# Kernel optimization log

Measured on AMD Instinct MI355X. Metric: run time of the kernel, lower is better.

The kernel has to match this reference:

```python
import jax, jax.numpy as jnp
import numpy as np
from itertools import product

C_IN, C_OUT = 32, 64
L, T = 96, 8            # 4D grid: 96^3 spatial x 8 time
EPS = 1e-5


def _build_maps():
    """Build sparse coords and MinkowskiEngine-style kernel maps (numpy, host side)."""
    rng = np.random.default_rng(0)
    n_cand = 400000
    coords = np.stack([rng.integers(0, L, n_cand), rng.integers(0, L, n_cand),
                       rng.integers(0, L, n_cand), rng.integers(0, T, n_cand)], axis=1).astype(np.int64)
    coords = np.unique(coords, axis=0)          # [n_in, 4] unique occupied voxels
    n_in = coords.shape[0]
    # --- downsample conv: kernel_size == stride == 2 -> each input hits exactly one output
    out_coords, inv = np.unique(coords // 2, axis=0, return_inverse=True)
    n_down = out_coords.shape[0]
    off_id = ((coords[:, 0] & 1) << 3) | ((coords[:, 1] & 1) << 2) | ((coords[:, 2] & 1) << 1) | (coords[:, 3] & 1)
    g, s = [], []
    for k in range(16):
        idx = np.nonzero(off_id == k)[0]
        g.append(idx); s.append(inv[idx])
    md = max(len(a) for a in g)
    gather_d = np.full((16, md), n_in, np.int32)    # dummy -> zero pad row of input feats
    scatter_d = np.full((16, md), n_down, np.int32)  # dummy -> trash output row
    for k in range(16):
        gather_d[k, :len(g[k])] = g[k]; scatter_d[k, :len(s[k])] = s[k]
    # --- refine conv: kernel 3, stride 1 on downsampled grid (same in/out coords)
    d0, d1 = L // 2, T // 2
    def enc(c):
        return ((c[:, 0] * d0 + c[:, 1]) * d0 + c[:, 2]) * d1 + c[:, 3]
    keys = enc(out_coords)
    order = np.argsort(keys)
    skeys = keys[order]
    g, s = [], []
    for off in product((-1, 0, 1), repeat=4):
        nb = out_coords + np.asarray(off)
        ok = (nb >= 0).all(1) & (nb[:, :3] < d0).all(1) & (nb[:, 3] < d1)
        nk = enc(np.where(ok[:, None], nb, 0))
        pos = np.clip(np.searchsorted(skeys, nk), 0, n_down - 1)
        hit = ok & (skeys[pos] == nk)
        g.append(order[pos[hit]]); s.append(np.nonzero(hit)[0])
    mr = max(len(a) for a in g)
    gather_r = np.full((81, mr), n_down, np.int32)
    scatter_r = np.full((81, mr), n_down, np.int32)
    for k in range(81):
        gather_r[k, :len(g[k])] = g[k]; scatter_r[k, :len(s[k])] = s[k]
    return n_in, n_down, gather_d, scatter_d, gather_r, scatter_r


def setup_inputs() -> dict:
    n_in, n_down, gather_d, scatter_d, gather_r, scatter_r = _build_maps()
    ks = jax.random.split(jax.random.key(0), 12)
    feat = jax.random.normal(ks[0], (n_in, C_IN), jnp.float32)
    w_down = jax.random.normal(ks[1], (16, C_IN, C_OUT), jnp.float32) / np.float32(np.sqrt(16 * C_IN))
    w_ref = jax.random.normal(ks[2], (81, C_OUT, C_OUT), jnp.float32) / np.float32(np.sqrt(81 * C_OUT))
    gamma_d = jnp.abs(jax.random.normal(ks[3], (C_OUT,), jnp.float32)) + 0.5
    beta_d = jax.random.normal(ks[4], (C_OUT,), jnp.float32) * 0.1
    mean_d = jax.random.normal(ks[5], (C_OUT,), jnp.float32) * 0.1
    var_d = jax.random.uniform(ks[6], (C_OUT,), jnp.float32, 0.5, 1.5)
    gamma_r = jnp.abs(jax.random.normal(ks[7], (C_OUT,), jnp.float32)) + 0.5
    beta_r = jax.random.normal(ks[8], (C_OUT,), jnp.float32) * 0.1
    mean_r = jax.random.normal(ks[9], (C_OUT,), jnp.float32) * 0.1
    var_r = jax.random.uniform(ks[10], (C_OUT,), jnp.float32, 0.5, 1.5)
    return {"feat": feat, "w_down": w_down, "gamma_d": gamma_d, "beta_d": beta_d,
            "mean_d": mean_d, "var_d": var_d, "w_ref": w_ref, "gamma_r": gamma_r,
            "beta_r": beta_r, "mean_r": mean_r, "var_r": var_r,
            "gather_d": jnp.asarray(gather_d), "scatter_d": jnp.asarray(scatter_d),
            "gather_r": jnp.asarray(gather_r), "scatter_r": jnp.asarray(scatter_r),
            "n_down": int(n_down)}


def _spconv_bn_relu(feat, w, gather, scatter, n_out, gamma, beta, mean, var):
    # gather-GEMM-scatter sparse conv, then eval-mode BN, then ReLU
    featp = jnp.concatenate([feat, jnp.zeros((1, feat.shape[1]), feat.dtype)], axis=0)
    out = jnp.zeros((n_out + 1, w.shape[-1]), feat.dtype)
    for k in range(w.shape[0]):        # fixed small set of kernel offsets (16 or 81)
        out = out.at[scatter[k]].add(featp[gather[k]] @ w[k])
    inv = gamma * jax.lax.rsqrt(var + EPS)
    return jax.nn.relu(out[:n_out] * inv + (beta - mean * inv))


def reference(feat, w_down, gamma_d, beta_d, mean_d, var_d, w_ref, gamma_r, beta_r,
              mean_r, var_r, gather_d, scatter_d, gather_r, scatter_r, n_down):
    n_down = int(n_down)
    y = _spconv_bn_relu(feat, w_down, gather_d, scatter_d, n_down, gamma_d, beta_d, mean_d, var_d)
    y = _spconv_bn_relu(y, w_ref, gather_r, scatter_r, n_down, gamma_r, beta_r, mean_r, var_r)
    return y
```

## Files before the change

kernel.cpp:

```cpp
#include <hip/hip_runtime.h>
#include <hip/hip_bf16.h>
#include <cstdint>

#define EPS_BN 1e-5f

typedef __attribute__((ext_vector_type(8)))  short bf16x8;
typedef __attribute__((ext_vector_type(16))) float f32x16;
typedef __attribute__((ext_vector_type(4)))  unsigned short u16x4;

#define MFMA32(a, b, c) __builtin_amdgcn_mfma_f32_32x32x16_bf16(a, b, c, 0, 0, 0)

#define GLOAD_LDS16(gsrc, ldst) \
    __builtin_amdgcn_global_load_lds((const __attribute__((address_space(1))) void*)(gsrc), \
                                     (__attribute__((address_space(3))) void*)(ldst), 16, 0, 0)

__global__ void build_inv(const int* __restrict__ gather, const int* __restrict__ scatter,
                          long total, int m, int* __restrict__ invT, int n_down) {
    long i = (long)blockIdx.x * blockDim.x + threadIdx.x;
    if (i >= total) return;
    int s = scatter[i];
    if (s < n_down) {
        int k = (int)(i / m);
        invT[(long)k * n_down + s] = gather[i];
    }
}

__global__ void build_invP(const int* __restrict__ gather, const int* __restrict__ scatter,
                           long total, int m, int* __restrict__ invP, int n_down, int nb64) {
    long i = (long)blockIdx.x * blockDim.x + threadIdx.x;
    if (i >= total) return;
    int s = scatter[i];
    if (s < n_down) {
        int k = (int)(i / m);
        int r = s & 63;
        int pos = ((r >> 5) << 5) + ((r & 7) << 2) + ((r >> 3) & 3);
        invP[(size_t)k * nb64 + ((size_t)(s >> 6) << 6) + pos] = gather[i];
    }
}

__global__ void fcvt(const float* __restrict__ f, unsigned short* __restrict__ fb,
                     unsigned short* __restrict__ ybf_pad, long n_in) {
    long t = (long)blockIdx.x * blockDim.x + threadIdx.x;
    long e = t * 4;
    long total = n_in * 32;
    if (e < total) {
        float4 v = *(const float4*)(f + e);
        u16x4 o;
        __hip_bfloat16 h;
        h = __float2bfloat16(v.x); o.x = *(unsigned short*)&h;
        h = __float2bfloat16(v.y); o.y = *(unsigned short*)&h;
        h = __float2bfloat16(v.z); o.z = *(unsigned short*)&h;
        h = __float2bfloat16(v.w); o.w = *(unsigned short*)&h;
        *(u16x4*)(fb + e) = o;
    } else if (e < total + 32) {
        u16x4 z = {0, 0, 0, 0};
        *(u16x4*)(fb + e) = z;
    }
    if (blockIdx.x == 0 && threadIdx.x < 16) {
        u16x4 z = {0, 0, 0, 0};
        ((u16x4*)ybf_pad)[threadIdx.x] = z;
    }
}

__global__ void wcvt_r(const float* __restrict__ w, unsigned short* __restrict__ wt) {
    int e = blockIdx.x * 256 + threadIdx.x;
    int k = e >> 12, r = e & 4095;
    int cin = ((r >> 10) << 4) + (r & 15);
    int col = (r >> 4) & 63;
    __hip_bfloat16 h = __float2bfloat16(w[(k << 12) + (cin << 6) + col]);
    wt[e] = *(unsigned short*)&h;
}

__global__ void wcvt_d(const float* __restrict__ w, unsigned short* __restrict__ wt) {
    int e = blockIdx.x * 256 + threadIdx.x;
    int k = e >> 11, r = e & 2047;
    int cin = ((r >> 10) << 4) + (r & 15);
    int col = (r >> 4) & 63;
    __hip_bfloat16 h = __float2bfloat16(w[(k << 11) + (cin << 6) + col]);
    wt[e] = *(unsigned short*)&h;
}

__global__ __launch_bounds__(256, 4) void conv_down_mfma(
        const unsigned short* __restrict__ fb, const unsigned short* __restrict__ wtd,
        const int* __restrict__ invd,
        const float* __restrict__ gamma, const float* __restrict__ beta,
        const float* __restrict__ mean, const float* __restrict__ var,
        unsigned short* __restrict__ y, int n_down, int n_in) {
    int  tid  = threadIdx.x;
    int  lane = tid & 63, l31 = lane & 31, lhi = lane >> 5;
    long wv   = ((long)blockIdx.x * 256 + tid) >> 6;
    long o0   = wv * 32;
    if (o0 >= n_down) return;

    int  oA = (int)(o0 + l31 < n_down ? o0 + l31 : n_down - 1);
    const short* ysb = (const short*)fb;

#define LDI_D(k) invd[(size_t)(k) * n_down + oA]
#define GATH_D(dst, g) { \
        const short* p = ysb + (size_t)((g) < 0 ? n_in : (g)) * 32 + lhi * 8; \
        dst[0] = *(const bf16x8*)p; dst[1] = *(const bf16x8*)(p + 16); }

    int g0 = LDI_D(0), gq1 = LDI_D(1), gq2 = LDI_D(2);
    bf16x8 ac[2];
    GATH_D(ac, g0);
    f32x16 acc0 = {}, acc1 = {};
    const short* wp = (const short*)wtd + l31 * 16 + lhi * 8;

    for (int k = 0; k < 16; ++k) {
        int gN = (k < 13) ? LDI_D(k + 3) : -1;
        bf16x8 an[2];
        GATH_D(an, gq1);
        const short* wk = wp + k * 2048;
#pragma unroll
        for (int kq = 0; kq < 2; ++kq) {
            bf16x8 b0 = *(const bf16x8*)(wk + kq * 1024);
            bf16x8 b1 = *(const bf16x8*)(wk + kq * 1024 + 512);
            acc0 = MFMA32(ac[kq], b0, acc0);
            acc1 = MFMA32(ac[kq], b1, acc1);
        }
        ac[0] = an[0]; ac[1] = an[1];
        gq1 = gq2; gq2 = gN;
    }

#pragma unroll
    for (int n = 0; n < 2; ++n) {
        int col = n * 32 + l31;
        float iv = gamma[col] * rsqrtf(var[col] + EPS_BN);
        float bb = beta[col] - mean[col] * iv;
        const f32x16& A = n ? acc1 : acc0;
#pragma unroll
        for (int i = 0; i < 16; ++i) {
            long oo = o0 + (i & 3) + 8 * (i >> 2) + 4 * lhi;
            if (oo < n_down) {
                __hip_bfloat16 h = __float2bfloat16(fmaxf(A[i] * iv + bb, 0.f));
                y[oo * 64 + col] = *(unsigned short*)&h;
            }
        }
    }
#undef LDI_D
#undef GATH_D
}

__global__ __launch_bounds__(256, 2) void conv_ref_mfma(
        const unsigned short* __restrict__ ybf, const unsigned short* __restrict__ wt,
        const int* __restrict__ invP,
        const float* __restrict__ gamma, const float* __restrict__ beta,
        const float* __restrict__ mean, const float* __restrict__ var,
        float* __restrict__ out, int n_down, int nb64, int nwg) {
    __shared__ char ldsA[4][2][8192];

    int bid = blockIdx.x;
    int q = nwg >> 3, r = nwg & 7;
    int xcd = bid & 7, pos = bid >> 3;
    int swzb = (xcd < r ? xcd * (q + 1) : r * (q + 1) + (xcd - r) * q) + pos;

    const int tid  = threadIdx.x;
    const int lane = tid & 63, l31 = lane & 31, lhi = lane >> 5;
    const int wid  = tid >> 6;
    const long o0  = ((long)swzb * 4 + wid) * 64;
    if (o0 >= n_down) return;

    const int  ro    = lane >> 3;
    const char* ybase = (const char*)ybf;
    char* ldsw = &ldsA[wid][0][0];
    const int swz = (((lane & 7) ^ ro) << 4);

    const char* ibase = (const char*)invP + (size_t)o0 * 4 + (size_t)ro * 16;

#define IDXP(k, S) { const char* p_ = ibase + (size_t)(k) * ((size_t)nb64 * 4); \
        S##a = *(const int4*)p_; S##b = *(const int4*)(p_ + 128); }

#define GL1(qv, BUF, i) { size_t g_ = (size_t)((qv) < 0 ? n_down : (qv)); \
        GLOAD_LDS16(ybase + g_ * 128 + swz, ldsw + (BUF) * 8192 + (i) * 1024); }

#define STAGE(BUF, S) { \
        GL1(S##a.x, BUF, 0); GL1(S##a.y, BUF, 1); GL1(S##a.z, BUF, 2); GL1(S##a.w, BUF, 3); \
        GL1(S##b.x, BUF, 4); GL1(S##b.y, BUF, 5); GL1(S##b.z, BUF, 6); GL1(S##b.w, BUF, 7); }

#define LDB(B0, B1, k) { \
        const short* wk_ = wp + (size_t)(k) * 4096; \
        _Pragma("unroll") \
        for (int kq = 0; kq < 4; ++kq) { \
            B0[kq] = *(const bf16x8*)(wk_ + kq * 1024); \
            B1[kq] = *(const bf16x8*)(wk_ + kq * 1024 + 512); } }

    const int rsw   = (l31 & 7) << 4;
    const int rowA  = l31 * 128, rowB = (32 + l31) * 128;
    const int lhi16 = lhi * 16;

#define COMPUTE(BUF, B0, B1) { \
        const char* la = ldsw + (BUF) * 8192; \
        __builtin_amdgcn_s_setprio(1); \
        _Pragma("unroll") \
        for (int kq = 0; kq < 4; ++kq) { \
            int fo = (kq * 32 + lhi16) ^ rsw; \
            bf16x8 aA = *(const bf16x8*)(la + rowA + fo); \
            bf16x8 aB = *(const bf16x8*)(la + rowB + fo); \
            acc0 = MFMA32(aA, B0[kq], acc0); \
            acc1 = MFMA32(aA, B1[kq], acc1); \
            acc2 = MFMA32(aB, B0[kq], acc2); \
            acc3 = MFMA32(aB, B1[kq], acc3); } \
        __builtin_amdgcn_s_setprio(0); }

#define REGION(CUR, NXT, S, kk, BC0, BC1, BN0, BN1) { \
        STAGE(NXT, S); \
        LDB(BN0, BN1, (kk) + 1); \
        IDXP((kk) + 4, S); \
        asm volatile("s_waitcnt vmcnt(20)" ::: "memory"); \
        __builtin_amdgcn_sched_barrier(0); \
        COMPUTE(CUR, BC0, BC1); }

    f32x16 acc0 = {}, acc1 = {}, acc2 = {}, acc3 = {};
    const short* wp = (const short*)wt + l31 * 16 + lhi * 8;
    bf16x8 B00[4], B01[4], B10[4], B11[4];
    int4 Ta, Tb, S0a, S0b, S1a, S1b, S2a, S2b;

    IDXP(0, T);
    IDXP(1, S0);
    IDXP(2, S1);
    IDXP(3, S2);
    asm volatile("s_waitcnt vmcnt(6)" ::: "memory");
    __builtin_amdgcn_sched_barrier(0);
    STAGE(0, T);
    LDB(B00, B01, 0);

    for (int k = 0; k < 78; k += 6) {
        REGION(0, 1, S0, k + 0, B00, B01, B10, B11);
        REGION(1, 0, S1, k + 1, B10, B11, B00, B01);
        REGION(0, 1, S2, k + 2, B00, B01, B10, B11);
        REGION(1, 0, S0, k + 3, B10, B11, B00, B01);
        REGION(0, 1, S1, k + 4, B00, B01, B10, B11);
        REGION(1, 0, S2, k + 5, B10, B11, B00, B01);
    }
    REGION(0, 1, S0, 78, B00, B01, B10, B11);
    REGION(1, 0, S1, 79, B10, B11, B00, B01);
    asm volatile("s_waitcnt vmcnt(2)" ::: "memory");
    __builtin_amdgcn_sched_barrier(0);
    COMPUTE(0, B00, B01);

#pragma unroll
    for (int m = 0; m < 2; ++m)
#pragma unroll
        for (int n = 0; n < 2; ++n) {
            int col = n * 32 + l31;
            float iv = gamma[col] * rsqrtf(var[col] + EPS_BN);
            float bb = beta[col] - mean[col] * iv;
            const f32x16& A = m == 0 ? (n == 0 ? acc0 : acc1) : (n == 0 ? acc2 : acc3);
#pragma unroll
            for (int i = 0; i < 16; ++i) {
                long oo = o0 + m * 32 + (i & 3) + 8 * (i >> 2) + 4 * lhi;
                if (oo < n_down)
                    out[oo * 64 + col] = fmaxf(A[i] * iv + bb, 0.f);
            }
        }
#undef IDXP
#undef GL1
#undef STAGE
#undef LDB
#undef COMPUTE
#undef REGION
}

extern "C" void kernel_launch(void* const* d_in, const int* in_sizes, int n_args,
                              void* d_out, int out_size, void* d_ws, size_t ws_size,
                              hipStream_t stream) {
    const float* feat    = (const float*)d_in[0];
    const float* w_down  = (const float*)d_in[1];
    const float* gamma_d = (const float*)d_in[2];
    const float* beta_d  = (const float*)d_in[3];
    const float* mean_d  = (const float*)d_in[4];
    const float* var_d   = (const float*)d_in[5];
    const float* w_ref   = (const float*)d_in[6];
    const float* gamma_r = (const float*)d_in[7];
    const float* beta_r  = (const float*)d_in[8];
    const float* mean_r  = (const float*)d_in[9];
    const float* var_r   = (const float*)d_in[10];
    const int*   gather_d  = (const int*)d_in[11];
    const int*   scatter_d = (const int*)d_in[12];
    const int*   gather_r  = (const int*)d_in[13];
    const int*   scatter_r = (const int*)d_in[14];

    int n_in   = in_sizes[0] / 32;
    int md     = in_sizes[11] / 16;
    int mr     = in_sizes[13] / 81;
    int n_down = out_size / 64;
    int nb64   = ((n_down + 63) / 64) * 64;

    char* ws = (char*)d_ws;
    size_t off = 0;
    auto alloc = [&](size_t bytes) { char* p = ws + off; off = (off + bytes + 255) & ~(size_t)255; return p; };
    unsigned short* ybf    = (unsigned short*)alloc((size_t)(n_down + 1) * 64 * 2);
    unsigned short* featbf = (unsigned short*)alloc((size_t)(n_in + 1) * 32 * 2);
    unsigned short* wt     = (unsigned short*)alloc((size_t)81 * 4096 * 2);
    unsigned short* wtd    = (unsigned short*)alloc((size_t)16 * 2048 * 2);
    int* invP = (int*)(ws + off);
    int* invd = invP + (size_t)84 * nb64;

    hipMemsetAsync(invP, 0xFF, ((size_t)84 * nb64 + (size_t)16 * n_down) * sizeof(int), stream);

    long td = 16L * md;
    build_inv<<<(int)((td + 255) / 256), 256, 0, stream>>>(gather_d, scatter_d, td, md, invd, n_down);
    long tr = 81L * mr;
    build_invP<<<(int)((tr + 255) / 256), 256, 0, stream>>>(gather_r, scatter_r, tr, mr, invP, n_down, nb64);

    long ft = ((long)n_in * 32 + 32) / 4;
    fcvt<<<(int)((ft + 255) / 256), 256, 0, stream>>>(feat, featbf, ybf + (size_t)n_down * 64, n_in);
    wcvt_r<<<81 * 4096 / 256, 256, 0, stream>>>(w_ref, wt);
    wcvt_d<<<16 * 2048 / 256, 256, 0, stream>>>(w_down, wtd);

    long wavesD  = ((long)n_down + 31) / 32;
    int  blocksD = (int)((wavesD * 64 + 255) / 256);
    conv_down_mfma<<<blocksD, 256, 0, stream>>>(featbf, wtd, invd,
                                                gamma_d, beta_d, mean_d, var_d,
                                                ybf, n_down, n_in);

    int blocksR = (n_down + 255) / 256;
    conv_ref_mfma<<<blocksR, 256, 0, stream>>>(ybf, wt, invP,
                                               gamma_r, beta_r, mean_r, var_r,
                                               (float*)d_out, n_down, nb64, blocksR);
}
```

Before: 403.9 us.

## Widen refine-conv wave tile to 128 rows and drop B double-buffering

Each wave of the refine conv now handles 128 output rows instead of 64, so every weight fragment loaded from global memory feeds eight MFMAs instead of four. Blocks shrink to two waves with larger per-wave LDS buffers, and the index permutation layout moves to 128-row groups. The weight register double-buffer is removed: weights for the next offset are loaded after compute rather than prefetched, which trims register pressure to make room for twice the accumulators. The tradeoff is less latency hiding on weight loads, fewer waves per CU, and a changed vmcnt accounting that now must cover 16 gathers per stage.

```diff
diff --git a/kernel.cpp b/kernel.cpp
--- a/kernel.cpp
+++ b/kernel.cpp
@@ -26,15 +26,15 @@
 }
 
 __global__ void build_invP(const int* __restrict__ gather, const int* __restrict__ scatter,
-                           long total, int m, int* __restrict__ invP, int n_down, int nb64) {
+                           long total, int m, int* __restrict__ invP, int n_down, int nb128) {
     long i = (long)blockIdx.x * blockDim.x + threadIdx.x;
     if (i >= total) return;
     int s = scatter[i];
     if (s < n_down) {
         int k = (int)(i / m);
-        int r = s & 63;
+        int r = s & 127;
         int pos = ((r >> 5) << 5) + ((r & 7) << 2) + ((r >> 3) & 3);
-        invP[(size_t)k * nb64 + ((size_t)(s >> 6) << 6) + pos] = gather[i];
+        invP[(size_t)k * nb128 + ((size_t)(s >> 7) << 7) + pos] = gather[i];
     }
 }
 
@@ -141,13 +141,13 @@
 #undef GATH_D
 }
 
-__global__ __launch_bounds__(256, 2) void conv_ref_mfma(
+__global__ __launch_bounds__(128, 1) void conv_ref_mfma(
         const unsigned short* __restrict__ ybf, const unsigned short* __restrict__ wt,
         const int* __restrict__ invP,
         const float* __restrict__ gamma, const float* __restrict__ beta,
         const float* __restrict__ mean, const float* __restrict__ var,
-        float* __restrict__ out, int n_down, int nb64, int nwg) {
-    __shared__ char ldsA[4][2][8192];
+        float* __restrict__ out, int n_down, int nb128, int nwg) {
+    __shared__ char ldsA[2][2][16384];
 
     int bid = blockIdx.x;
     int q = nwg >> 3, r = nwg & 7;
@@ -157,7 +157,7 @@
     const int tid  = threadIdx.x;
     const int lane = tid & 63, l31 = lane & 31, lhi = lane >> 5;
     const int wid  = tid >> 6;
-    const long o0  = ((long)swzb * 4 + wid) * 64;
+    const long o0  = ((long)swzb * 2 + wid) * 128;
     if (o0 >= n_down) return;
 
     const int  ro    = lane >> 3;
@@ -167,17 +167,20 @@
 
     const char* ibase = (const char*)invP + (size_t)o0 * 4 + (size_t)ro * 16;
 
-#define IDXP(k, S) { const char* p_ = ibase + (size_t)(k) * ((size_t)nb64 * 4); \
-        S##a = *(const int4*)p_; S##b = *(const int4*)(p_ + 128); }
+#define IDXP(k, S) { const char* p_ = ibase + (size_t)(k) * ((size_t)nb128 * 4); \
+        S##a = *(const int4*)p_;         S##b = *(const int4*)(p_ + 128); \
+        S##c = *(const int4*)(p_ + 256); S##d = *(const int4*)(p_ + 384); }
 
 #define GL1(qv, BUF, i) { size_t g_ = (size_t)((qv) < 0 ? n_down : (qv)); \
-        GLOAD_LDS16(ybase + g_ * 128 + swz, ldsw + (BUF) * 8192 + (i) * 1024); }
+        GLOAD_LDS16(ybase + g_ * 128 + swz, ldsw + (BUF) * 16384 + (i) * 1024); }
 
 #define STAGE(BUF, S) { \
-        GL1(S##a.x, BUF, 0); GL1(S##a.y, BUF, 1); GL1(S##a.z, BUF, 2); GL1(S##a.w, BUF, 3); \
-        GL1(S##b.x, BUF, 4); GL1(S##b.y, BUF, 5); GL1(S##b.z, BUF, 6); GL1(S##b.w, BUF, 7); }
-
-#define LDB(B0, B1, k) { \
+        GL1(S##a.x, BUF, 0);  GL1(S##a.y, BUF, 1);  GL1(S##a.z, BUF, 2);  GL1(S##a.w, BUF, 3); \
+        GL1(S##b.x, BUF, 4);  GL1(S##b.y, BUF, 5);  GL1(S##b.z, BUF, 6);  GL1(S##b.w, BUF, 7); \
+        GL1(S##c.x, BUF, 8);  GL1(S##c.y, BUF, 9);  GL1(S##c.z, BUF, 10); GL1(S##c.w, BUF, 11); \
+        GL1(S##d.x, BUF, 12); GL1(S##d.y, BUF, 13); GL1(S##d.z, BUF, 14); GL1(S##d.w, BUF, 15); }
+
+#define LDB(k) { \
         const short* wk_ = wp + (size_t)(k) * 4096; \
         _Pragma("unroll") \
         for (int kq = 0; kq < 4; ++kq) { \
@@ -185,72 +188,68 @@
             B1[kq] = *(const bf16x8*)(wk_ + kq * 1024 + 512); } }
 
     const int rsw   = (l31 & 7) << 4;
-    const int rowA  = l31 * 128, rowB = (32 + l31) * 128;
     const int lhi16 = lhi * 16;
 
-#define COMPUTE(BUF, B0, B1) { \
-        const char* la = ldsw + (BUF) * 8192; \
+#define COMPUTE(BUF) { \
+        const char* la = ldsw + (BUF) * 16384; \
         __builtin_amdgcn_s_setprio(1); \
         _Pragma("unroll") \
         for (int kq = 0; kq < 4; ++kq) { \
             int fo = (kq * 32 + lhi16) ^ rsw; \
-            bf16x8 aA = *(const bf16x8*)(la + rowA + fo); \
-            bf16x8 aB = *(const bf16x8*)(la + rowB + fo); \
-            acc0 = MFMA32(aA, B0[kq], acc0); \
-            acc1 = MFMA32(aA, B1[kq], acc1); \
-            acc2 = MFMA32(aB, B0[kq], acc2); \
-            acc3 = MFMA32(aB, B1[kq], acc3); } \
+            _Pragma("unroll") \
+            for (int m = 0; m < 4; ++m) { \
+                bf16x8 a_ = *(const bf16x8*)(la + m * 4096 + l31 * 128 + fo); \
+                acc[m][0] = MFMA32(a_, B0[kq], acc[m][0]); \
+                acc[m][1] = MFMA32(a_, B1[kq], acc[m][1]); } } \
         __builtin_amdgcn_s_setprio(0); }
 
-#define REGION(CUR, NXT, S, kk, BC0, BC1, BN0, BN1) { \
-        STAGE(NXT, S); \
-        LDB(BN0, BN1, (kk) + 1); \
-        IDXP((kk) + 4, S); \
+#define REGION(CUR, NXT, SS, SL, kk) { \
+        STAGE(NXT, SS); \
+        IDXP((kk) + 3, SL); \
         asm volatile("s_waitcnt vmcnt(20)" ::: "memory"); \
         __builtin_amdgcn_sched_barrier(0); \
-        COMPUTE(CUR, BC0, BC1); }
-
-    f32x16 acc0 = {}, acc1 = {}, acc2 = {}, acc3 = {};
+        COMPUTE(CUR); \
+        LDB((kk) + 1); }
+
+    f32x16 acc[4][2] = {};
     const short* wp = (const short*)wt + l31 * 16 + lhi * 8;
-    bf16x8 B00[4], B01[4], B10[4], B11[4];
-    int4 Ta, Tb, S0a, S0b, S1a, S1b, S2a, S2b;
-
-    IDXP(0, T);
-    IDXP(1, S0);
-    IDXP(2, S1);
-    IDXP(3, S2);
-    asm volatile("s_waitcnt vmcnt(6)" ::: "memory");
+    bf16x8 B0[4], B1[4];
+    int4 S0a, S0b, S0c, S0d, S1a, S1b, S1c, S1d, S2a, S2b, S2c, S2d;
+
+    IDXP(0, S0);
+    IDXP(1, S1);
+    IDXP(2, S2);
+    asm volatile("s_waitcnt vmcnt(8)" ::: "memory");
     __builtin_amdgcn_sched_barrier(0);
-    STAGE(0, T);
-    LDB(B00, B01, 0);
+    STAGE(0, S0);
+    LDB(0);
 
     for (int k = 0; k < 78; k += 6) {
-        REGION(0, 1, S0, k + 0, B00, B01, B10, B11);
-        REGION(1, 0, S1, k + 1, B10, B11, B00, B01);
-        REGION(0, 1, S2, k + 2, B00, B01, B10, B11);
-        REGION(1, 0, S0, k + 3, B10, B11, B00, B01);
-        REGION(0, 1, S1, k + 4, B00, B01, B10, B11);
-        REGION(1, 0, S2, k + 5, B10, B11, B00, B01);
-    }
-    REGION(0, 1, S0, 78, B00, B01, B10, B11);
-    REGION(1, 0, S1, 79, B10, B11, B00, B01);
-    asm volatile("s_waitcnt vmcnt(2)" ::: "memory");
+        REGION(0, 1, S1, S0, k + 0);
+        REGION(1, 0, S2, S1, k + 1);
+        REGION(0, 1, S0, S2, k + 2);
+        REGION(1, 0, S1, S0, k + 3);
+        REGION(0, 1, S2, S1, k + 4);
+        REGION(1, 0, S0, S2, k + 5);
+    }
+    REGION(0, 1, S1, S0, 78);
+    REGION(1, 0, S2, S1, 79);
+    asm volatile("s_waitcnt vmcnt(0)" ::: "memory");
     __builtin_amdgcn_sched_barrier(0);
-    COMPUTE(0, B00, B01);
-
-#pragma unroll
-    for (int m = 0; m < 2; ++m)
+    COMPUTE(0);
+
+#pragma unroll
+    for (int m = 0; m < 4; ++m)
 #pragma unroll
         for (int n = 0; n < 2; ++n) {
             int col = n * 32 + l31;
             float iv = gamma[col] * rsqrtf(var[col] + EPS_BN);
             float bb = beta[col] - mean[col] * iv;
-            const f32x16& A = m == 0 ? (n == 0 ? acc0 : acc1) : (n == 0 ? acc2 : acc3);
 #pragma unroll
             for (int i = 0; i < 16; ++i) {
                 long oo = o0 + m * 32 + (i & 3) + 8 * (i >> 2) + 4 * lhi;
                 if (oo < n_down)
-                    out[oo * 64 + col] = fmaxf(A[i] * iv + bb, 0.f);
+                    out[oo * 64 + col] = fmaxf(acc[m][n][i] * iv + bb, 0.f);
             }
         }
 #undef IDXP
@@ -284,7 +283,7 @@
     int md     = in_sizes[11] / 16;
     int mr     = in_sizes[13] / 81;
     int n_down = out_size / 64;
-    int nb64   = ((n_down + 63) / 64) * 64;
+    int nb128  = ((n_down + 127) / 128) * 128;
 
     char* ws = (char*)d_ws;
     size_t off = 0;
@@ -294,14 +293,14 @@
     unsigned short* wt     = (unsigned short*)alloc((size_t)81 * 4096 * 2);
     unsigned short* wtd    = (unsigned short*)alloc((size_t)16 * 2048 * 2);
     int* invP = (int*)(ws + off);
-    int* invd = invP + (size_t)84 * nb64;
-
-    hipMemsetAsync(invP, 0xFF, ((size_t)84 * nb64 + (size_t)16 * n_down) * sizeof(int), stream);
+    int* invd = invP + (size_t)84 * nb128;
+
+    hipMemsetAsync(invP, 0xFF, ((size_t)84 * nb128 + (size_t)16 * n_down) * sizeof(int), stream);
 
     long td = 16L * md;
     build_inv<<<(int)((td + 255) / 256), 256, 0, stream>>>(gather_d, scatter_d, td, md, invd, n_down);
     long tr = 81L * mr;
-    build_invP<<<(int)((tr + 255) / 256), 256, 0, stream>>>(gather_r, scatter_r, tr, mr, invP, n_down, nb64);
+    build_invP<<<(int)((tr + 255) / 256), 256, 0, stream>>>(gather_r, scatter_r, tr, mr, invP, n_down, nb128);
 
     long ft = ((long)n_in * 32 + 32) / 4;
     fcvt<<<(int)((ft + 255) / 256), 256, 0, stream>>>(feat, featbf, ybf + (size_t)n_down * 64, n_in);
@@ -315,7 +314,7 @@
                                                 ybf, n_down, n_in);
 
     int blocksR = (n_down + 255) / 256;
-    conv_ref_mfma<<<blocksR, 256, 0, stream>>>(ybf, wt, invP,
+    conv_ref_mfma<<<blocksR, 128, 0, stream>>>(ybf, wt, invP,
                                                gamma_r, beta_r, mean_r, var_r,
-                                               (float*)d_out, n_down, nb64, blocksR);
-}
+                                               (float*)d_out, n_down, nb128, blocksR);
+}
```

Result: slower. 494.7 us (+22.5%).
